# Kernel tuning notes

Hardware: AMD Instinct MI355X
Metric: run time of the kernel (lower is better)

## Reference

```python
import jax, jax.numpy as jnp
import numpy as np

HIDDEN = 2048
HEADS = 16
HEAD_DIM = HIDDEN // HEADS
TOP_K = 256
B, N = 1, 2048


def setup_inputs() -> dict:
    key = jax.random.key(0)
    ks = jax.random.split(key, 9)
    s = 0.02
    return {
        "hidden_states": jax.random.normal(ks[0], (B, N, HIDDEN), jnp.float32),
        "Wq": jax.random.normal(ks[1], (HIDDEN, HIDDEN), jnp.float32) * s,
        "bq": jnp.zeros((HIDDEN,), jnp.float32),
        "Wk": jax.random.normal(ks[2], (HIDDEN, HIDDEN), jnp.float32) * s,
        "bk": jnp.zeros((HIDDEN,), jnp.float32),
        "Wv": jax.random.normal(ks[3], (HIDDEN, HIDDEN), jnp.float32) * s,
        "bv": jnp.zeros((HIDDEN,), jnp.float32),
        "Wo": jax.random.normal(ks[4], (HIDDEN, HIDDEN), jnp.float32) * s,
        "bo": jnp.zeros((HIDDEN,), jnp.float32),
    }


def _split_heads(x):
    b, n, _ = x.shape
    return x.reshape(b, n, HEADS, HEAD_DIM).transpose(0, 2, 1, 3)  # b h n d


def reference(hidden_states, Wq, bq, Wk, bk, Wv, bv, Wo, bo):
    scale = 1.0 / jnp.sqrt(jnp.float32(HEAD_DIM))
    q = _split_heads(hidden_states @ Wq + bq)  # [b,h,n,d]
    k = _split_heads(hidden_states @ Wk + bk)
    v = _split_heads(hidden_states @ Wv + bv)

    # Sparse path (kv_seq_length > attention_window): dense QK^T used only to rank keys.
    scores = jnp.einsum("bhnd,bhmd->bhnm", q, k) * scale  # [b,h,n,n]
    importance = scores.mean(axis=2)  # [b,h,n] aggregate over queries
    _, idx = jax.lax.top_k(importance, TOP_K)  # [b,h,k]

    # gather selected K/V (torch.gather along seq dim)
    k_sel = jnp.take_along_axis(k, idx[..., None], axis=2)  # [b,h,k,d]
    v_sel = jnp.take_along_axis(v, idx[..., None], axis=2)

    w = jax.nn.softmax(jnp.einsum("bhnd,bhkd->bhnk", q, k_sel) * scale, axis=-1)
    out = jnp.einsum("bhnk,bhkd->bhnd", w, v_sel)  # [b,h,n,d]
    out = out.transpose(0, 2, 1, 3).reshape(hidden_states.shape[0], -1, HIDDEN)
    return out @ Wo + bo
```

## Files before the change

### kernel.cpp

```cpp
#include <hip/hip_runtime.h>


typedef __attribute__((ext_vector_type(8))) short bf16x8;
typedef __attribute__((ext_vector_type(4))) float f32x4;

__device__ __forceinline__ unsigned short f2bf(float x) {
    unsigned u = __float_as_uint(x);
    u += 0x7fffu + ((u >> 16) & 1u);
    return (unsigned short)(u >> 16);
}

__device__ __forceinline__ void load_lds16(const unsigned short* g, unsigned short* l) {
    __builtin_amdgcn_global_load_lds(
        (const __attribute__((address_space(1))) unsigned int*)g,
        (__attribute__((address_space(3))) unsigned int*)l,
        16, 0, 0);
}

struct Ptr4  { const float* p[4]; };

__global__ __launch_bounds__(256) void gemm_qkv(
    const unsigned short* __restrict__ HSb,
    const unsigned short* __restrict__ WT4,
    const float* __restrict__ bq,
    const float* __restrict__ bk,
    const float* __restrict__ bv,
    const int* __restrict__ idx,
    unsigned short* __restrict__ Qb,
    unsigned short* __restrict__ Ksel,
    unsigned short* __restrict__ VselT)
{
    __shared__ __align__(16) unsigned short As[128][32];
    __shared__ __align__(16) unsigned short Bs[128][32];

    const int tid  = threadIdx.x;
    const int lane = tid & 63;
    const int wave = tid >> 6;
    const int wm = wave >> 1, wn = wave & 1;
    const int lr = lane >> 2;
    const int lc = (lane & 3) * 8;

    const int bid = blockIdx.x;

    int kv, h = 0, bm, bn;
    const unsigned short* Bt;
    long ar0, ar1;
    if (bid < 64) {
        kv = 1 + (bid >> 5);
        const int t = bid & 31;
        h  = t >> 1;
        bm = (t & 1) * 128;
        bn = h * 128;
        Bt = WT4 + (long)kv * 4194304;
        ar0 = idx[h * 256 + bm + wave * 16 + lr];
        ar1 = idx[h * 256 + bm + wave * 16 + 64 + lr];
    } else {
        kv = 0;
        const int t = bid - 64;
        bm = (t >> 4) * 128;
        bn = (t & 15) * 128;
        Bt = WT4;
        ar0 = bm + wave * 16 + lr;
        ar1 = bm + wave * 16 + 64 + lr;
    }

    f32x4 acc[4][4];
#pragma unroll
    for (int i = 0; i < 4; i++)
#pragma unroll
        for (int j = 0; j < 4; j++) acc[i][j] = f32x4{0.f, 0.f, 0.f, 0.f};

    for (int k0 = 0; k0 < 2048; k0 += 32) {
        __syncthreads();
        const int r0 = wave * 16;
        load_lds16(HSb + ar0 * 2048 + k0 + lc, &As[r0][0]);
        load_lds16(Bt + (long)(bn + r0 + lr) * 2048 + k0 + lc, &Bs[r0][0]);
        load_lds16(HSb + ar1 * 2048 + k0 + lc, &As[r0 + 64][0]);
        load_lds16(Bt + (long)(bn + r0 + 64 + lr) * 2048 + k0 + lc, &Bs[r0 + 64][0]);
        __syncthreads();

        bf16x8 af[4], bf[4];
#pragma unroll
        for (int s = 0; s < 4; s++)
            af[s] = *(const bf16x8*)&As[wm * 64 + s * 16 + (lane & 15)][(lane >> 4) * 8];
#pragma unroll
        for (int t = 0; t < 4; t++)
            bf[t] = *(const bf16x8*)&Bs[wn * 64 + t * 16 + (lane & 15)][(lane >> 4) * 8];
#pragma unroll
        for (int s = 0; s < 4; s++)
#pragma unroll
            for (int t = 0; t < 4; t++)
                acc[s][t] = __builtin_amdgcn_mfma_f32_16x16x32_bf16(af[s], bf[t], acc[s][t], 0, 0, 0);
    }

    if (kv == 0) {
#pragma unroll
        for (int s = 0; s < 4; s++) {
#pragma unroll
            for (int t = 0; t < 4; t++) {
                const int col  = bn + wn * 64 + t * 16 + (lane & 15);
                const int row0 = bm + wm * 64 + s * 16 + (lane >> 4) * 4;
                const float bb = bq[col];
#pragma unroll
                for (int r = 0; r < 4; r++)
                    Qb[(long)(row0 + r) * 2048 + col] = f2bf(acc[s][t][r] + bb);
            }
        }
    } else {
        const float* bp = (kv == 1) ? bk : bv;
#pragma unroll
        for (int s = 0; s < 4; s++) {
#pragma unroll
            for (int t = 0; t < 4; t++) {
                const int col = bn + wn * 64 + t * 16 + (lane & 15);
                const int dd  = col & 127;
                const float bb = bp[col];
                const int j0 = bm + wm * 64 + s * 16 + (lane >> 4) * 4;
#pragma unroll
                for (int r = 0; r < 4; r++) {
                    const int j = j0 + r;
                    const unsigned short h16 = f2bf(acc[s][t][r] + bb);
                    if (kv == 1) Ksel [h * 32768 + j * 128 + dd] = h16;
                    else         VselT[h * 32768 + dd * 256 + j] = h16;
                }
            }
        }
    }
}

__global__ __launch_bounds__(256) void gemm_o(
    const unsigned short* __restrict__ Att,
    const unsigned short* __restrict__ WoT,
    float* __restrict__ Opart)
{
    __shared__ __align__(16) unsigned short As[128][32];
    __shared__ __align__(16) unsigned short Bs[128][32];

    const int tid  = threadIdx.x;
    const int lane = tid & 63;
    const int wave = tid >> 6;
    const int wm = wave >> 1, wn = wave & 1;
    const int lr = lane >> 2;
    const int lc = (lane & 3) * 8;

    const int bm = blockIdx.y * 128;
    const int bn = blockIdx.x * 128;
    const int b  = blockIdx.z;

    const unsigned short* Ab = Att + b * 1024;
    const unsigned short* Bb = WoT + b * 1024;

    f32x4 acc[4][4];
#pragma unroll
    for (int i = 0; i < 4; i++)
#pragma unroll
        for (int j = 0; j < 4; j++) acc[i][j] = f32x4{0.f, 0.f, 0.f, 0.f};

    for (int k0 = 0; k0 < 1024; k0 += 32) {
        __syncthreads();
#pragma unroll
        for (int r0 = wave * 16; r0 < 128; r0 += 64) {
            load_lds16(Ab + (long)(bm + r0 + lr) * 2048 + k0 + lc, &As[r0][0]);
            load_lds16(Bb + (long)(bn + r0 + lr) * 2048 + k0 + lc, &Bs[r0][0]);
        }
        __syncthreads();

        bf16x8 af[4], bf[4];
#pragma unroll
        for (int s = 0; s < 4; s++)
            af[s] = *(const bf16x8*)&As[wm * 64 + s * 16 + (lane & 15)][(lane >> 4) * 8];
#pragma unroll
        for (int t = 0; t < 4; t++)
            bf[t] = *(const bf16x8*)&Bs[wn * 64 + t * 16 + (lane & 15)][(lane >> 4) * 8];
#pragma unroll
        for (int s = 0; s < 4; s++)
#pragma unroll
            for (int t = 0; t < 4; t++)
                acc[s][t] = __builtin_amdgcn_mfma_f32_16x16x32_bf16(af[s], bf[t], acc[s][t], 0, 0, 0);
    }

#pragma unroll
    for (int s = 0; s < 4; s++) {
#pragma unroll
        for (int t = 0; t < 4; t++) {
            const int col  = bn + wn * 64 + t * 16 + (lane & 15);
            const int row0 = bm + wm * 64 + s * 16 + (lane >> 4) * 4;
#pragma unroll
            for (int r = 0; r < 4; r++)
                Opart[(long)b * 4194304 + (long)(row0 + r) * 2048 + col] = acc[s][t][r];
        }
    }
}

__global__ __launch_bounds__(256) void oreduce(const float* __restrict__ part,
                                               const float* __restrict__ bo,
                                               float* __restrict__ out) {
    const long i = ((long)blockIdx.x * 256 + threadIdx.x) * 4;
    float4 a = *(const float4*)(part + i);
    float4 b = *(const float4*)(part + 4194304 + i);
    const int col = (int)(i & 2047);
    float4 o;
    o.x = a.x + b.x + bo[col];
    o.y = a.y + b.y + bo[col + 1];
    o.z = a.z + b.z + bo[col + 2];
    o.w = a.w + b.w + bo[col + 3];
    *(float4*)(out + i) = o;
}

#define QS_OFF(c)  ((c) * 2048)
#define KS_OFF(c)  (4096 + (c) * 8192)
#define PS_OFF     0
#define VS_OFF(c)  (16896 + (c) * 4096)

__global__ __launch_bounds__(256, 2) void attn_kernel(
    const unsigned short* __restrict__ Qb,
    const unsigned short* __restrict__ Ksel,
    const unsigned short* __restrict__ VselT,
    unsigned short* __restrict__ Att)
{
    __shared__ __align__(16) unsigned short smem[25088];
    __shared__ float linv[64];

    const int tid  = threadIdx.x;
    const int lane = tid & 63;
    const int wave = tid >> 6;
    const int bm = blockIdx.x * 64;
    const int h  = blockIdx.y;
    const int lr = lane >> 2, lc = (lane & 3) * 8;

    const unsigned short* Kh = Ksel  + h * 32768;
    const unsigned short* Vh = VselT + h * 32768;

    f32x4 acc[16];
#pragma unroll
    for (int t = 0; t < 16; t++) acc[t] = f32x4{0.f, 0.f, 0.f, 0.f};

#pragma unroll
    for (int c2 = 0; c2 < 2; c2++) {
        __syncthreads();
#pragma unroll
        for (int c = 0; c < 2; c++) {
            const int k0 = c2 * 64 + c * 32;
            load_lds16(Qb + (long)(bm + wave * 16 + lr) * 2048 + h * 128 + k0 + lc,
                       &smem[QS_OFF(c) + wave * 512]);
#pragma unroll
            for (int q = 0; q < 4; q++)
                load_lds16(Kh + (wave * 64 + q * 16 + lr) * 128 + k0 + lc,
                           &smem[KS_OFF(c) + (wave * 64 + q * 16) * 32]);
        }
        __syncthreads();
#pragma unroll
        for (int kk = 0; kk < 2; kk++) {
            bf16x8 af = *(const bf16x8*)&smem[QS_OFF(kk) + (wave * 16 + (lane & 15)) * 32 + (lane >> 4) * 8];
#pragma unroll
            for (int t = 0; t < 16; t++) {
                bf16x8 bfv = *(const bf16x8*)&smem[KS_OFF(kk) + (t * 16 + (lane & 15)) * 32 + (lane >> 4) * 8];
                acc[t] = __builtin_amdgcn_mfma_f32_16x16x32_bf16(af, bfv, acc[t], 0, 0, 0);
            }
        }
    }
    __syncthreads();

    const float se = 0.08838834764831845f * 1.4426950408889634f;
#pragma unroll
    for (int r = 0; r < 4; r++) {
        float mx = -3.0e38f;
#pragma unroll
        for (int t = 0; t < 16; t++) mx = fmaxf(mx, acc[t][r]);
#pragma unroll
        for (int off = 1; off < 16; off <<= 1) mx = fmaxf(mx, __shfl_xor(mx, off));
        float sum = 0.f;
#pragma unroll
        for (int t = 0; t < 16; t++) {
            float p = exp2f((acc[t][r] - mx) * se);
            acc[t][r] = p;
            sum += p;
        }
#pragma unroll
        for (int off = 1; off < 16; off <<= 1) sum += __shfl_xor(sum, off);
        const int row = wave * 16 + (lane >> 4) * 4 + r;
#pragma unroll
        for (int t = 0; t < 16; t++)
            smem[PS_OFF + row * 264 + t * 16 + (lane & 15)] = f2bf(acc[t][r]);
        if ((lane & 15) == 0) linv[row] = 1.0f / sum;
    }

    const int wm2 = wave >> 1, wn2 = wave & 1;
    f32x4 acc2[2][4];
#pragma unroll
    for (int i = 0; i < 2; i++)
#pragma unroll
        for (int j = 0; j < 4; j++) acc2[i][j] = f32x4{0.f, 0.f, 0.f, 0.f};

#pragma unroll
    for (int c2 = 0; c2 < 4; c2++) {
#pragma unroll
        for (int c = 0; c < 2; c++) {
            const int j0 = c2 * 64 + c * 32;
#pragma unroll
            for (int q = 0; q < 2; q++)
                load_lds16(Vh + (wave * 32 + q * 16 + lr) * 256 + j0 + lc,
                           &smem[VS_OFF(c) + (wave * 32 + q * 16) * 32]);
        }
        __syncthreads();
#pragma unroll
        for (int c = 0; c < 2; c++) {
            const int j0 = c2 * 64 + c * 32;
            bf16x8 af2[2], bf2v[4];
#pragma unroll
            for (int s2 = 0; s2 < 2; s2++)
                af2[s2] = *(const bf16x8*)&smem[PS_OFF + (wm2 * 32 + s2 * 16 + (lane & 15)) * 264 + j0 + (lane >> 4) * 8];
#pragma unroll
            for (int t2 = 0; t2 < 4; t2++)
                bf2v[t2] = *(const bf16x8*)&smem[VS_OFF(c) + (wn2 * 64 + t2 * 16 + (lane & 15)) * 32 + (lane >> 4) * 8];
#pragma unroll
            for (int s2 = 0; s2 < 2; s2++)
#pragma unroll
                for (int t2 = 0; t2 < 4; t2++)
                    acc2[s2][t2] = __builtin_amdgcn_mfma_f32_16x16x32_bf16(af2[s2], bf2v[t2], acc2[s2][t2], 0, 0, 0);
        }
        __syncthreads();
    }

#pragma unroll
    for (int s2 = 0; s2 < 2; s2++) {
#pragma unroll
        for (int t2 = 0; t2 < 4; t2++) {
            const int d = wn2 * 64 + t2 * 16 + (lane & 15);
#pragma unroll
            for (int r = 0; r < 4; r++) {
                const int row = wm2 * 32 + s2 * 16 + (lane >> 4) * 4 + r;
                float v = acc2[s2][t2][r] * linv[row];
                Att[(long)(bm + row) * 2048 + h * 128 + d] = f2bf(v);
            }
        }
    }
}

__global__ __launch_bounds__(256) void prep_kernel(Ptr4 srcs, unsigned short* __restrict__ WT4,
                                                   const float* __restrict__ hs,
                                                   double* __restrict__ part) {
    const int b = blockIdx.x;
    const int tid = threadIdx.x;
    if (b < 4096) {
        __shared__ float tile[64][65];
        const int z = b >> 10, xy = b & 1023;
        const float* W = srcs.p[z];
        unsigned short* WT = WT4 + (long)z * 4194304;
        const int bx = (xy & 31) * 64;
        const int by = (xy >> 5) * 64;
        const int x = tid & 63, y = tid >> 6;
#pragma unroll
        for (int i = 0; i < 64; i += 4)
            tile[y + i][x] = W[(long)(by + y + i) * 2048 + bx + x];
        __syncthreads();
#pragma unroll
        for (int i = 0; i < 64; i += 4)
            WT[(long)(bx + y + i) * 2048 + by + x] = f2bf(tile[x][y + i]);
    } else {
        const int c = b - 4096;
        const int col = (c & 7) * 256 + tid;
        const int r0  = (c >> 3) * 32;
        double a = 0.0;
#pragma unroll 4
        for (int r = 0; r < 32; r++) a += (double)hs[(long)(r0 + r) * 2048 + col];
        part[(long)(c >> 3) * 2048 + col] = a;
    }
}

__global__ void fill_kernel(float* p, float v, long n) {
    long i = ((long)blockIdx.x * blockDim.x + threadIdx.x) * 4;
    if (i + 3 < n) { p[i] = v; p[i+1] = v; p[i+2] = v; p[i+3] = v; }
}

__global__ __launch_bounds__(256) void mean_qsum_part(const double* __restrict__ part,
                                                      const float* __restrict__ Wq,
                                                      double* __restrict__ partq) {
    __shared__ float hsb[32];
    const int j  = blockIdx.x * 256 + threadIdx.x;
    const int i0 = blockIdx.y * 32;
    if (threadIdx.x < 32) {
        double s = 0.0;
#pragma unroll 4
        for (int g = 0; g < 64; g++) s += part[(long)g * 2048 + i0 + threadIdx.x];
        hsb[threadIdx.x] = (float)(s * (1.0 / 2048.0));
    }
    __syncthreads();
    double a = 0.0;
#pragma unroll 4
    for (int r = 0; r < 32; r++)
        a += (double)hsb[r] * (double)Wq[(long)(i0 + r) * 2048 + j];
    partq[(long)blockIdx.y * 2048 + j] = a;
}

__global__ void qsum_fin(const double* __restrict__ partq, const float* __restrict__ bq,
                         float* __restrict__ qbar) {
    const int j = blockIdx.x * 64 + threadIdx.x;
    double s = (double)bq[j];
#pragma unroll 4
    for (int g = 0; g < 64; g++) s += partq[(long)g * 2048 + j];
    qbar[j] = (float)s;
}

__global__ __launch_bounds__(256) void u_kernel(const float* __restrict__ Wk,
                                                const float* __restrict__ qbar,
                                                float* __restrict__ U) {
    const int i = blockIdx.x, t = threadIdx.x;
#pragma unroll
    for (int r = 0; r < 2; r++) {
        const int e = r * 1024 + t * 4;
        float4 w = *(const float4*)(Wk + (long)i * 2048 + e);
        float4 q = *(const float4*)(qbar + e);
        float a = w.x * q.x + w.y * q.y + w.z * q.z + w.w * q.w;
#pragma unroll
        for (int off = 16; off; off >>= 1) a += __shfl_xor(a, off);
        if ((t & 31) == 0) U[(long)i * 16 + r * 8 + (t >> 5)] = a;
    }
}

__global__ __launch_bounds__(256) void cast_imp_kernel(const float* __restrict__ hs,
                                                       const float* __restrict__ U,
                                                       unsigned short* __restrict__ HSb,
                                                       float* __restrict__ imp) {
    __shared__ float row[2048];
    __shared__ float red[4][16];
    const int m = blockIdx.x, t = threadIdx.x;
    for (int i = t; i < 2048; i += 256) {
        float v = hs[(long)m * 2048 + i];
        row[i] = v;
        HSb[(long)m * 2048 + i] = f2bf(v);
    }
    __syncthreads();
    float p[16];
#pragma unroll
    for (int h = 0; h < 16; h++) p[h] = 0.f;
    for (int i = t * 8; i < t * 8 + 8; i++) {
        const float v = row[i];
        const float* u = U + i * 16;
#pragma unroll
        for (int h = 0; h < 16; h++) p[h] += v * u[h];
    }
#pragma unroll
    for (int off = 32; off; off >>= 1)
#pragma unroll
        for (int h = 0; h < 16; h++) p[h] += __shfl_down(p[h], off);
    if ((t & 63) == 0)
#pragma unroll
        for (int h = 0; h < 16; h++) red[t >> 6][h] = p[h];
    __syncthreads();
    if (t < 16)
        imp[(long)t * 2048 + m] = red[0][t] + red[1][t] + red[2][t] + red[3][t];
}

__global__ __launch_bounds__(64) void topk_idx(const float* __restrict__ imp,
                                               int* __restrict__ idx) {
    const int h = blockIdx.x;
    const int lane = threadIdx.x;
    unsigned u[32];
#pragma unroll
    for (int r = 0; r < 32; r++) {
        unsigned x = __float_as_uint(imp[(long)h * 2048 + r * 64 + lane]);
        u[r] = (x & 0x80000000u) ? ~x : (x | 0x80000000u);
    }
    unsigned cur = 0;
    for (int b = 31; b >= 0; b--) {
        const unsigned cand = cur | (1u << b);
        int tot = 0;
#pragma unroll
        for (int r = 0; r < 32; r++)
            tot += (int)__popcll(__ballot(u[r] >= cand));
        if (tot >= 256) cur = cand;
    }
    const unsigned long long below = (1ull << lane) - 1ull;
    int pos[32];
    int base = 0;
#pragma unroll
    for (int r = 0; r < 32; r++) {
        const bool q = u[r] > cur;
        const unsigned long long m = __ballot(q);
        pos[r] = q ? base + (int)__popcll(m & below) : -1;
        base += (int)__popcll(m);
    }
#pragma unroll
    for (int r = 0; r < 32; r++) {
        const bool q = (u[r] == cur);
        const unsigned long long m = __ballot(q);
        if (q) {
            const int p = base + (int)__popcll(m & below);
            pos[r] = (p < 256) ? p : -1;
        }
        base += (int)__popcll(m);
    }
#pragma unroll
    for (int r = 0; r < 32; r++)
        if (pos[r] >= 0) idx[h * 256 + pos[r]] = r * 64 + lane;
}

extern "C" void kernel_launch(void* const* d_in, const int* in_sizes, int n_in,
                              void* d_out, int out_size, void* d_ws, size_t ws_size,
                              hipStream_t stream)
{
    const float* hs = (const float*)d_in[0];
    const float* Wq = (const float*)d_in[1];
    const float* bq = (const float*)d_in[2];
    const float* Wk = (const float*)d_in[3];
    const float* bk = (const float*)d_in[4];
    const float* Wv = (const float*)d_in[5];
    const float* bv = (const float*)d_in[6];
    const float* Wo = (const float*)d_in[7];
    const float* bo = (const float*)d_in[8];

    char* ws = (char*)d_ws;
    size_t off = 0;
    auto alloc = [&](size_t b) -> void* {
        void* p = ws + off;
        off = (off + b + 255) & ~(size_t)255;
        return p;
    };
    unsigned short* HSb   = (unsigned short*)alloc(8388608);
    unsigned short* WT4   = (unsigned short*)alloc(4 * 8388608);
    unsigned short* Qb    = (unsigned short*)alloc(8388608);
    unsigned short* Att   = (unsigned short*)alloc(8388608);
    unsigned short* Ksel  = (unsigned short*)alloc(1048576);
    unsigned short* VselT = (unsigned short*)alloc(1048576);
    float* Opart = (float*)alloc(2 * 16777216);
    double* part  = (double*)alloc(1048576);
    double* partq = (double*)alloc(1048576);
    float* qbar  = (float*)alloc(8192);
    float* U     = (float*)alloc(131072);
    float* imp   = (float*)alloc(131072);
    int*   idx   = (int*)alloc(16384);

    if (off > ws_size) {
        fill_kernel<<<4096, 256, 0, stream>>>((float*)d_out, 12345.0f, (long)out_size);
        return;
    }

    unsigned short* WoT = WT4 + 3 * 4194304;

    prep_kernel<<<4608, 256, 0, stream>>>(Ptr4{{Wq, Wk, Wv, Wo}}, WT4, hs, part);

    mean_qsum_part<<<dim3(8, 64), 256, 0, stream>>>(part, Wq, partq);
    qsum_fin<<<32, 64, 0, stream>>>(partq, bq, qbar);
    u_kernel<<<2048, 256, 0, stream>>>(Wk, qbar, U);
    cast_imp_kernel<<<2048, 256, 0, stream>>>(hs, U, HSb, imp);

    topk_idx<<<16, 64, 0, stream>>>(imp, idx);

    gemm_qkv<<<320, 256, 0, stream>>>(HSb, WT4, bq, bk, bv, idx, Qb, Ksel, VselT);

    attn_kernel<<<dim3(32, 16), 256, 0, stream>>>(Qb, Ksel, VselT, Att);

    gemm_o<<<dim3(16, 16, 2), 256, 0, stream>>>(Att, WoT, Opart);

    oreduce<<<4096, 256, 0, stream>>>(Opart, bo, (float*)d_out);
}
```

Baseline: 321.0 us.

## Double-buffer LDS tiles in QKV and output GEMMs, swizzle Q tile order

Both GEMM kernels now use two LDS buffers: the next K-slice is issued with global_load_lds before the current slice's MFMAs run, so there is one barrier per step instead of two and global-load latency overlaps compute. The Q-projection blocks are remapped into 4x4 groups of tiles to improve L2 reuse of the activation and weight rows. Row base pointers are hoisted out of the loop. LDS per block doubles, and correctness depends on the barrier placement keeping the buffer being refilled separate from the one being read.

```diff
diff --git a/kernel.cpp b/kernel.cpp
--- a/kernel.cpp
+++ b/kernel.cpp
@@ -30,8 +30,8 @@
     unsigned short* __restrict__ Ksel,
     unsigned short* __restrict__ VselT)
 {
-    __shared__ __align__(16) unsigned short As[128][32];
-    __shared__ __align__(16) unsigned short Bs[128][32];
+    __shared__ __align__(16) unsigned short As[2][128][32];
+    __shared__ __align__(16) unsigned short Bs[2][128][32];
 
     const int tid  = threadIdx.x;
     const int lane = tid & 63;
@@ -57,12 +57,18 @@
     } else {
         kv = 0;
         const int t = bid - 64;
-        bm = (t >> 4) * 128;
-        bn = (t & 15) * 128;
+        const int st = t >> 4, u = t & 15;
+        bm = ((st >> 2) * 4 + (u >> 2)) * 128;
+        bn = ((st & 3) * 4 + (u & 3)) * 128;
         Bt = WT4;
         ar0 = bm + wave * 16 + lr;
-        ar1 = bm + wave * 16 + 64 + lr;
-    }
+        ar1 = ar0 + 64;
+    }
+
+    const unsigned short* Arow0 = HSb + ar0 * 2048 + lc;
+    const unsigned short* Arow1 = HSb + ar1 * 2048 + lc;
+    const unsigned short* Brow0 = Bt + (long)(bn + wave * 16 + lr) * 2048 + lc;
+    const unsigned short* Brow1 = Brow0 + 64 * 2048;
 
     f32x4 acc[4][4];
 #pragma unroll
@@ -70,27 +76,37 @@
 #pragma unroll
         for (int j = 0; j < 4; j++) acc[i][j] = f32x4{0.f, 0.f, 0.f, 0.f};
 
-    for (int k0 = 0; k0 < 2048; k0 += 32) {
-        __syncthreads();
-        const int r0 = wave * 16;
-        load_lds16(HSb + ar0 * 2048 + k0 + lc, &As[r0][0]);
-        load_lds16(Bt + (long)(bn + r0 + lr) * 2048 + k0 + lc, &Bs[r0][0]);
-        load_lds16(HSb + ar1 * 2048 + k0 + lc, &As[r0 + 64][0]);
-        load_lds16(Bt + (long)(bn + r0 + 64 + lr) * 2048 + k0 + lc, &Bs[r0 + 64][0]);
-        __syncthreads();
-
+    auto stage = [&](int b, int k0) {
+        load_lds16(Arow0 + k0, &As[b][wave * 16][0]);
+        load_lds16(Brow0 + k0, &Bs[b][wave * 16][0]);
+        load_lds16(Arow1 + k0, &As[b][wave * 16 + 64][0]);
+        load_lds16(Brow1 + k0, &Bs[b][wave * 16 + 64][0]);
+    };
+    auto compute = [&](int b) {
         bf16x8 af[4], bf[4];
 #pragma unroll
         for (int s = 0; s < 4; s++)
-            af[s] = *(const bf16x8*)&As[wm * 64 + s * 16 + (lane & 15)][(lane >> 4) * 8];
+            af[s] = *(const bf16x8*)&As[b][wm * 64 + s * 16 + (lane & 15)][(lane >> 4) * 8];
 #pragma unroll
         for (int t = 0; t < 4; t++)
-            bf[t] = *(const bf16x8*)&Bs[wn * 64 + t * 16 + (lane & 15)][(lane >> 4) * 8];
+            bf[t] = *(const bf16x8*)&Bs[b][wn * 64 + t * 16 + (lane & 15)][(lane >> 4) * 8];
 #pragma unroll
         for (int s = 0; s < 4; s++)
 #pragma unroll
             for (int t = 0; t < 4; t++)
                 acc[s][t] = __builtin_amdgcn_mfma_f32_16x16x32_bf16(af[s], bf[t], acc[s][t], 0, 0, 0);
+    };
+
+    stage(0, 0);
+    for (int t = 0; t < 64; t += 2) {
+        __syncthreads();
+        stage(1, (t + 1) * 32);
+        asm volatile("" ::: "memory");
+        compute(0);
+        __syncthreads();
+        if (t + 2 < 64) stage(0, (t + 2) * 32);
+        asm volatile("" ::: "memory");
+        compute(1);
     }
 
     if (kv == 0) {
@@ -133,8 +149,8 @@
     const unsigned short* __restrict__ WoT,
     float* __restrict__ Opart)
 {
-    __shared__ __align__(16) unsigned short As[128][32];
-    __shared__ __align__(16) unsigned short Bs[128][32];
+    __shared__ __align__(16) unsigned short As[2][128][32];
+    __shared__ __align__(16) unsigned short Bs[2][128][32];
 
     const int tid  = threadIdx.x;
     const int lane = tid & 63;
@@ -147,8 +163,10 @@
     const int bn = blockIdx.x * 128;
     const int b  = blockIdx.z;
 
-    const unsigned short* Ab = Att + b * 1024;
-    const unsigned short* Bb = WoT + b * 1024;
+    const unsigned short* Arow0 = Att + b * 1024 + (long)(bm + wave * 16 + lr) * 2048 + lc;
+    const unsigned short* Arow1 = Arow0 + 64 * 2048;
+    const unsigned short* Brow0 = WoT + b * 1024 + (long)(bn + wave * 16 + lr) * 2048 + lc;
+    const unsigned short* Brow1 = Brow0 + 64 * 2048;
 
     f32x4 acc[4][4];
 #pragma unroll
@@ -156,27 +174,37 @@
 #pragma unroll
         for (int j = 0; j < 4; j++) acc[i][j] = f32x4{0.f, 0.f, 0.f, 0.f};
 
-    for (int k0 = 0; k0 < 1024; k0 += 32) {
-        __syncthreads();
-#pragma unroll
-        for (int r0 = wave * 16; r0 < 128; r0 += 64) {
-            load_lds16(Ab + (long)(bm + r0 + lr) * 2048 + k0 + lc, &As[r0][0]);
-            load_lds16(Bb + (long)(bn + r0 + lr) * 2048 + k0 + lc, &Bs[r0][0]);
-        }
-        __syncthreads();
-
+    auto stage = [&](int bb, int k0) {
+        load_lds16(Arow0 + k0, &As[bb][wave * 16][0]);
+        load_lds16(Brow0 + k0, &Bs[bb][wave * 16][0]);
+        load_lds16(Arow1 + k0, &As[bb][wave * 16 + 64][0]);
+        load_lds16(Brow1 + k0, &Bs[bb][wave * 16 + 64][0]);
+    };
+    auto compute = [&](int bb) {
         bf16x8 af[4], bf[4];
 #pragma unroll
         for (int s = 0; s < 4; s++)
-            af[s] = *(const bf16x8*)&As[wm * 64 + s * 16 + (lane & 15)][(lane >> 4) * 8];
+            af[s] = *(const bf16x8*)&As[bb][wm * 64 + s * 16 + (lane & 15)][(lane >> 4) * 8];
 #pragma unroll
         for (int t = 0; t < 4; t++)
-            bf[t] = *(const bf16x8*)&Bs[wn * 64 + t * 16 + (lane & 15)][(lane >> 4) * 8];
+            bf[t] = *(const bf16x8*)&Bs[bb][wn * 64 + t * 16 + (lane & 15)][(lane >> 4) * 8];
 #pragma unroll
         for (int s = 0; s < 4; s++)
 #pragma unroll
             for (int t = 0; t < 4; t++)
                 acc[s][t] = __builtin_amdgcn_mfma_f32_16x16x32_bf16(af[s], bf[t], acc[s][t], 0, 0, 0);
+    };
+
+    stage(0, 0);
+    for (int t = 0; t < 32; t += 2) {
+        __syncthreads();
+        stage(1, (t + 1) * 32);
+        asm volatile("" ::: "memory");
+        compute(0);
+        __syncthreads();
+        if (t + 2 < 32) stage(0, (t + 2) * 32);
+        asm volatile("" ::: "memory");
+        compute(1);
     }
 
 #pragma unroll
```

Result: no change. 323.3 us (+0.7%).
